# Kernel tuning notes

Measured on AMD Instinct MI355X. Metric: run time of the kernel, lower is better.

The kernel has to match this reference:

```python
import jax, jax.numpy as jnp
import numpy as np

N, E, G = 50000, 800000, 128          # nodes, edges, graphs
L, T, F = 4, 4, 20                    # conv layers, towers, per-tower width
D = T * F                             # 80 = hidden dim
EDGE_DIM = 16
AVG_DEG_LOG = float(np.log(17.0))     # avg_deg['log'] for avg in-degree ~16
EPS_STD = 1e-5
EPS_BN = 1e-5


def setup_inputs() -> dict:
    ks = iter(jax.random.split(jax.random.key(0), 32))
    rn = lambda *s: jax.random.normal(next(ks), s, jnp.float32) * 0.1
    return dict(
        x=jax.random.randint(next(ks), (N, 9), 0, 16),
        edge_index=jax.random.randint(next(ks), (2, E), 0, N),
        batch=jnp.sort(jax.random.randint(next(ks), (N,), 0, G)),
        edge_attr=rn(E, EDGE_DIM),
        atom_emb=rn(9, 16, D),
        edge_w=rn(L, EDGE_DIM, F), edge_b=jnp.zeros((L, F), jnp.float32),
        pre_w1=rn(L, T, 3 * F, F), pre_b1=jnp.zeros((L, T, F), jnp.float32),
        pre_w2=rn(L, T, F, F), pre_b2=jnp.zeros((L, T, F), jnp.float32),
        post_w1=rn(L, T, 13 * F, F), post_b1=jnp.zeros((L, T, F), jnp.float32),
        post_w2=rn(L, T, F, F), post_b2=jnp.zeros((L, T, F), jnp.float32),
        lin_w=rn(L, D, D), lin_b=jnp.zeros((L, D), jnp.float32),
        bn_g=jnp.ones((L, D), jnp.float32), bn_b=jnp.zeros((L, D), jnp.float32),
        mlp_w1=rn(D, 40), mlp_b1=jnp.zeros(40, jnp.float32),
        mlp_w2=rn(40, 20), mlp_b2=jnp.zeros(20, jnp.float32),
        mlp_w3=rn(20, 1), mlp_b3=jnp.zeros(1, jnp.float32),
    )


def _net(x, edge_index, batch, edge_attr, atom_emb, edge_w, edge_b, pre_w1,
         pre_b1, pre_w2, pre_b2, post_w1, post_b1, post_w2, post_b2, lin_w,
         lin_b, bn_g, bn_b, mlp_w1, mlp_b1, mlp_w2, mlp_b2, mlp_w3, mlp_b3):
    src, dst = edge_index[0], edge_index[1]
    # AtomEncoder: sum of 9 categorical embeddings -> [N, D]
    h = atom_emb[jnp.arange(9)[None, :], x].sum(1)
    deg_raw = jax.ops.segment_sum(jnp.ones((E,), jnp.float32), dst, N)
    deg = jnp.clip(deg_raw, 1.0)
    has_edge = (deg_raw > 0)[:, None, None]
    d3 = deg[:, None, None]
    logd = jnp.log(deg + 1.0)[:, None, None]
    for l in range(L):  # 4 PNAConv + BN + ReLU + residual (dropout off / eval)
        xt = h.reshape(N, T, F)
        ea = edge_attr @ edge_w[l] + edge_b[l]                      # [E, F]
        # message: concat(x_i, x_j, edge) -> per-tower pre MLP
        m = jnp.concatenate([xt[dst], xt[src],
                             jnp.broadcast_to(ea[:, None, :], (E, T, F))], -1)
        m = jax.nn.relu(jnp.einsum('eti,tio->eto', m, pre_w1[l]) + pre_b1[l])
        m = jnp.einsum('eti,tio->eto', m, pre_w2[l]) + pre_b2[l]    # [E,T,F]
        # multi-aggregator scatter-reduce
        mean = jax.ops.segment_sum(m, dst, N) / d3
        msq = jax.ops.segment_sum(m * m, dst, N) / d3
        std = jnp.sqrt(jax.nn.relu(msq - mean * mean) + EPS_STD)
        mn = jnp.where(has_edge, jax.ops.segment_min(m, dst, N), 0.0)
        mx = jnp.where(has_edge, jax.ops.segment_max(m, dst, N), 0.0)
        agg = jnp.concatenate([mean, mn, mx, std], -1)              # [N,T,4F]
        # degree scalers: identity, amplification, attenuation
        out = jnp.concatenate([agg, agg * (logd / AVG_DEG_LOG),
                               agg * (AVG_DEG_LOG / logd)], -1)     # [N,T,12F]
        out = jnp.concatenate([xt, out], -1)                        # [N,T,13F]
        out = jax.nn.relu(jnp.einsum('nti,tio->nto', out, post_w1[l]) + post_b1[l])
        out = jnp.einsum('nti,tio->nto', out, post_w2[l]) + post_b2[l]
        out = out.reshape(N, D) @ lin_w[l] + lin_b[l]
        # BatchNorm over nodes (batch statistics)
        mu = out.mean(0)
        var = jnp.mean((out - mu) ** 2, axis=0)
        out = (out - mu) * (bn_g[l] / jnp.sqrt(var + EPS_BN)) + bn_b[l]
        h = jax.nn.relu(out) + h
    # global mean pool over graphs + readout MLP
    cnt = jnp.clip(jax.ops.segment_sum(jnp.ones((N,), jnp.float32), batch, G), 1.0)
    g = jax.ops.segment_sum(h, batch, G) / cnt[:, None]
    g = jax.nn.relu(g @ mlp_w1 + mlp_b1)
    g = jax.nn.relu(g @ mlp_w2 + mlp_b2)
    return g @ mlp_w3 + mlp_b3                                      # [G, 1]


def reference(x, edge_index, batch, edge_attr, atom_emb, edge_w, edge_b, pre_w1,
              pre_b1, pre_w2, pre_b2, post_w1, post_b1, post_w2, post_b2, lin_w,
              lin_b, bn_g, bn_b, mlp_w1, mlp_b1, mlp_w2, mlp_b2, mlp_w3, mlp_b3):
    return _net(x, edge_index, batch, edge_attr, atom_emb, edge_w, edge_b, pre_w1,
                pre_b1, pre_w2, pre_b2, post_w1, post_b1, post_w2, post_b2,
                lin_w, lin_b, bn_g, bn_b, mlp_w1, mlp_b1, mlp_w2, mlp_b2,
                mlp_w3, mlp_b3)
```

## Files before the change

### kernel.cpp

```cpp
#include <hip/hip_runtime.h>
#include <hip/hip_bf16.h>

#define NN 50000
#define EE 800000
#define GG 128
#define LL 4
#define TT 4
#define FF 20
#define DD 80
#define SCAN_B ((NN + 1023) / 1024)
static constexpr float AVG_LOG = 2.8332133440562162f;

typedef __fp16 half2v __attribute__((ext_vector_type(2)));

__device__ __forceinline__ float bf2f(unsigned short u) {
  return __uint_as_float((unsigned)u << 16);
}
__device__ __forceinline__ unsigned short f2bf(float f) {
  __hip_bfloat16 b = __float2bfloat16(f);
  return *(unsigned short*)&b;
}
__device__ __forceinline__ half2v pkrtz(float a, float b) {
#if __has_builtin(__builtin_amdgcn_cvt_pkrtz)
  return __builtin_amdgcn_cvt_pkrtz(a, b);
#else
  half2v h; h.x = (__fp16)a; h.y = (__fp16)b; return h;
#endif
}
__device__ __forceinline__ float fdot2(half2v a, half2v b, float c) {
#if __has_builtin(__builtin_amdgcn_fdot2)
  return __builtin_amdgcn_fdot2(a, b, c, false);
#else
  return fmaf((float)a.x, (float)b.x, fmaf((float)a.y, (float)b.y, c));
#endif
}
__device__ __forceinline__ half2v u2h2(unsigned int u) {
  return __builtin_bit_cast(half2v, u);
}
__device__ __forceinline__ unsigned int h22u(half2v h) {
  return __builtin_bit_cast(unsigned int, h);
}
__device__ __forceinline__ unsigned int packh2_rne(float a, float b) {
  half2v h; h.x = (__fp16)a; h.y = (__fp16)b;
  return h22u(h);
}
__device__ __forceinline__ unsigned int pack_bf16(float a, float b) {
  return (unsigned int)f2bf(a) | ((unsigned int)f2bf(b) << 16);
}

__global__ __launch_bounds__(256) void k_h(const int* __restrict__ x,
                                           const float* __restrict__ atom_emb,
                                           float* __restrict__ h) {
  int idx = blockIdx.x * 256 + threadIdx.x;
  if (idx >= NN * DD) return;
  int n = idx / DD, d = idx - n * DD;
  const int* xr = x + n * 9;
  float acc = 0.f;
#pragma unroll
  for (int i = 0; i < 9; ++i) {
    int v = xr[i];
    acc += atom_emb[(i * 16 + v) * DD + d];
  }
  h[idx] = acc;
}

__global__ __launch_bounds__(256) void k_deg(const int* __restrict__ ei, int* __restrict__ cnt) {
  int e = blockIdx.x * 256 + threadIdx.x;
  if (e >= EE) return;
  atomicAdd(&cnt[ei[EE + e]], 1);
}

__global__ __launch_bounds__(1024) void k_scan_sum(const int* __restrict__ cnt, int* __restrict__ bsum) {
  __shared__ int red[1024];
  int tid = threadIdx.x;
  int i = blockIdx.x * 1024 + tid;
  red[tid] = (i < NN) ? cnt[i] : 0;
  __syncthreads();
  for (int off = 512; off > 0; off >>= 1) {
    if (tid < off) red[tid] += red[tid + off];
    __syncthreads();
  }
  if (tid == 0) bsum[blockIdx.x] = red[0];
}

__global__ void k_scan_top(const int* __restrict__ bsum, int* __restrict__ boff,
                           int* __restrict__ row_ptr) {
  if (threadIdx.x == 0 && blockIdx.x == 0) {
    int acc = 0;
    for (int b = 0; b < SCAN_B; ++b) { boff[b] = acc; acc += bsum[b]; }
    row_ptr[NN] = acc;
  }
}

__global__ __launch_bounds__(1024) void k_scan_apply(const int* __restrict__ cnt,
                                                     const int* __restrict__ boff,
                                                     int* __restrict__ row_ptr,
                                                     int* __restrict__ cursor) {
  __shared__ int sm[1024];
  int tid = threadIdx.x;
  int i = blockIdx.x * 1024 + tid;
  int v = (i < NN) ? cnt[i] : 0;
  sm[tid] = v;
  __syncthreads();
  for (int off = 1; off < 1024; off <<= 1) {
    int t = (tid >= off) ? sm[tid - off] : 0;
    __syncthreads();
    sm[tid] += t;
    __syncthreads();
  }
  int excl = boff[blockIdx.x] + sm[tid] - v;
  if (i < NN) { row_ptr[i] = excl; cursor[i] = excl; }
}

__global__ __launch_bounds__(256) void k_csrfill(const int* __restrict__ ei,
                                                 int* __restrict__ cursor,
                                                 int2* __restrict__ csr2,
                                                 int* __restrict__ csr_dst) {
  int e = blockIdx.x * 256 + threadIdx.x;
  if (e >= EE) return;
  int dst = ei[EE + e];
  int slot = atomicAdd(&cursor[dst], 1);
  csr2[slot] = make_int2(ei[e], e);
  csr_dst[slot] = dst;
}

__global__ __launch_bounds__(256) void k_nodeparams(const int* __restrict__ cnt,
                                                    float* __restrict__ inv_deg,
                                                    float* __restrict__ s1a,
                                                    float* __restrict__ s2a) {
  int n = blockIdx.x * 256 + threadIdx.x;
  if (n >= NN) return;
  int c = cnt[n];
  float deg = (c > 0) ? (float)c : 1.0f;
  inv_deg[n] = 1.0f / deg;
  float logd = logf(deg + 1.0f);
  s1a[n] = logd / AVG_LOG;
  s2a[n] = AVG_LOG / logd;
}

__global__ __launch_bounds__(64) void k_wcomb(const float* __restrict__ edge_w,
                                              const float* __restrict__ edge_b,
                                              const float* __restrict__ pre_w1,
                                              const float* __restrict__ pre_b1,
                                              const float* __restrict__ pre_w2,
                                              unsigned int* __restrict__ wcpk,
                                              unsigned int* __restrict__ w2pk,
                                              float* __restrict__ biasc, int l) {
  int t = blockIdx.x;
  int wt = l * TT + t;
  const float* W1 = pre_w1 + (size_t)wt * 1200;
  const float* W2 = pre_w2 + (size_t)wt * 400;
  const float* ew = edge_w + (size_t)l * 16 * FF;
  const float* eb = edge_b + (size_t)l * FF;
  int j = threadIdx.x;
  if (j >= FF) return;
  float col[16];
  for (int i = 0; i < 16; ++i) {
    float acc = 0.f;
#pragma unroll
    for (int f = 0; f < FF; ++f) acc = fmaf(ew[i * FF + f], W1[(40 + f) * FF + j], acc);
    col[i] = acc;
  }
#pragma unroll
  for (int i2 = 0; i2 < 8; ++i2)
    wcpk[((size_t)t * FF + j) * 8 + i2] = packh2_rne(col[2 * i2], col[2 * i2 + 1]);
#pragma unroll
  for (int i2 = 0; i2 < 10; ++i2)
    w2pk[((size_t)t * FF + j) * 10 + i2] = packh2_rne(W2[(2 * i2) * FF + j], W2[(2 * i2 + 1) * FF + j]);
  float b = pre_b1[wt * FF + j];
#pragma unroll
  for (int f = 0; f < FF; ++f) b = fmaf(eb[f], W1[(40 + f) * FF + j], b);
  biasc[t * FF + j] = b;
}

__global__ __launch_bounds__(256) void k_prenode(
    const float* __restrict__ h, const float* __restrict__ pre_w1,
    const float* __restrict__ biasc,
    unsigned short* __restrict__ predD, unsigned short* __restrict__ predS, int l) {
  int tid = threadIdx.x;
  int t = tid >> 6, lane = tid & 63;
  int n = blockIdx.x * 64 + lane;
  if (n >= NN) return;
  int wt_u = __builtin_amdgcn_readfirstlane(l * TT + t);
  const float* W1 = pre_w1 + (size_t)wt_u * 1200;
  const float* bc = biasc + t * FF;
  float xt[FF];
  {
    const float4* pp = (const float4*)(h + (size_t)n * DD + t * FF);
#pragma unroll
    for (int i = 0; i < 5; ++i) { float4 v = pp[i]; xt[i*4]=v.x; xt[i*4+1]=v.y; xt[i*4+2]=v.z; xt[i*4+3]=v.w; }
  }
  float d[FF], s[FF];
#pragma unroll
  for (int j = 0; j < FF; ++j) { d[j] = bc[j]; s[j] = 0.f; }
#pragma unroll
  for (int i = 0; i < FF; ++i) {
    float a = xt[i];
#pragma unroll
    for (int j = 0; j < FF; ++j) {
      d[j] = fmaf(a, W1[i * FF + j], d[j]);
      s[j] = fmaf(a, W1[(FF + i) * FF + j], s[j]);
    }
  }
  ushort4* pd = (ushort4*)(predD + (size_t)n * DD + t * FF);
  ushort4* ps = (ushort4*)(predS + (size_t)n * DD + t * FF);
#pragma unroll
  for (int i = 0; i < 5; ++i) {
    pd[i] = make_ushort4(f2bf(d[i*4]), f2bf(d[i*4+1]), f2bf(d[i*4+2]), f2bf(d[i*4+3]));
    ps[i] = make_ushort4(f2bf(s[i*4]), f2bf(s[i*4+1]), f2bf(s[i*4+2]), f2bf(s[i*4+3]));
  }
}

__global__ __launch_bounds__(256, 4) void k_pre(
    const unsigned short* __restrict__ predD, const unsigned short* __restrict__ predS,
    const float* __restrict__ edge_attr,
    const int2* __restrict__ csr2, const int* __restrict__ csr_dst,
    const int* __restrict__ row_ptr,
    const unsigned int* __restrict__ wcpk,
    const unsigned int* __restrict__ w2pk,
    const float* __restrict__ pre_b2,
    unsigned int* __restrict__ m, int l, int n0, int n1, int capSlots) {
  int tid = threadIdx.x;
  int t = tid >> 6;
  int lane = tid & 63;
  int wt_u = __builtin_amdgcn_readfirstlane(l * TT + t);
  int t_u  = __builtin_amdgcn_readfirstlane(t);
  const unsigned int* Wcp = wcpk + (size_t)t_u * FF * 8;
  const unsigned int* W2p = w2pk + (size_t)t_u * FF * 10;
  const float* b2 = pre_b2 + (size_t)wt_u * FF;

  int sl = blockIdx.x * 64 + lane;
  int base = row_ptr[n0], end = row_ptr[n1];
  if (sl >= capSlots || base + sl >= end) return;
  int p = base + sl;
  int2 se = csr2[p];
  int dst = csr_dst[p];

  float m1[FF];
  {
    const ushort4* pp = (const ushort4*)(predD + (size_t)dst * DD + t * FF);
    const ushort4* qq = (const ushort4*)(predS + (size_t)se.x * DD + t * FF);
#pragma unroll
    for (int i = 0; i < 5; ++i) {
      ushort4 u = pp[i];
      ushort4 v = qq[i];
      m1[i*4+0] = bf2f(u.x) + bf2f(v.x);
      m1[i*4+1] = bf2f(u.y) + bf2f(v.y);
      m1[i*4+2] = bf2f(u.z) + bf2f(v.z);
      m1[i*4+3] = bf2f(u.w) + bf2f(v.w);
    }
  }
  half2v eap[8];
  {
    const float4* ap = (const float4*)(edge_attr + (size_t)se.y * 16);
#pragma unroll
    for (int i = 0; i < 4; ++i) {
      float4 v = ap[i];
      eap[2*i]   = pkrtz(v.x, v.y);
      eap[2*i+1] = pkrtz(v.z, v.w);
    }
  }
#pragma unroll
  for (int j = 0; j < FF; ++j) {
    float c = m1[j];
#pragma unroll
    for (int i2 = 0; i2 < 8; ++i2) c = fdot2(eap[i2], u2h2(Wcp[j * 8 + i2]), c);
    m1[j] = c;
  }
  half2v mp[10];
#pragma unroll
  for (int pr = 0; pr < 10; ++pr)
    mp[pr] = pkrtz(fmaxf(m1[2*pr], 0.f), fmaxf(m1[2*pr+1], 0.f));
  float m2[FF];
#pragma unroll
  for (int j = 0; j < FF; ++j) {
    float c = b2[j];
#pragma unroll
    for (int i2 = 0; i2 < 10; ++i2) c = fdot2(mp[i2], u2h2(W2p[j * 10 + i2]), c);
    m2[j] = c;
  }
  unsigned int* mrow = m + (size_t)t * 10 * capSlots + sl;
#pragma unroll
  for (int pr = 0; pr < 10; ++pr)
    mrow[(size_t)pr * capSlots] = h22u(pkrtz(m2[2*pr], m2[2*pr+1]));
}

__global__ __launch_bounds__(320) void k_agg(
    const unsigned int* __restrict__ m,
    const int* __restrict__ row_ptr,
    const float* __restrict__ inv_deg,
    unsigned short* __restrict__ aggbuf, int n0, int n1, int capSlots) {
  int tid = threadIdx.x;
  int t = blockIdx.x & 3, tile = blockIdx.x >> 2;
  int ni = tid / 10, pr = tid - ni * 10;
  int n = n0 + tile * 32 + ni;
  if (n >= n1) return;
  int base = row_ptr[n0];
  int beg = row_ptr[n], end = row_ptr[n + 1];
  float inv = inv_deg[n];
  int s0 = beg - base, s1c = end - base;
  if (s0 < 0) s0 = 0;
  if (s1c > capSlots) s1c = capSlots;
  float sum0 = 0.f, sum1 = 0.f, sq0 = 0.f, sq1 = 0.f;
  float mn0 = 3.4e38f, mn1 = 3.4e38f, mx0 = -3.4e38f, mx1 = -3.4e38f;
  const unsigned int* mrow = m + (size_t)(t * 10 + pr) * capSlots;
  int p = s0;
  for (; p < s1c && (p & 3); ++p) {
    half2v h = u2h2(mrow[p]);
    float v0 = (float)h.x, v1 = (float)h.y;
    sum0 += v0; sq0 = fmaf(v0, v0, sq0); mn0 = fminf(mn0, v0); mx0 = fmaxf(mx0, v0);
    sum1 += v1; sq1 = fmaf(v1, v1, sq1); mn1 = fminf(mn1, v1); mx1 = fmaxf(mx1, v1);
  }
  for (; p + 4 <= s1c; p += 4) {
    uint4 q = *(const uint4*)(mrow + p);
#pragma unroll
    for (int k = 0; k < 4; ++k) {
      unsigned int u = (k == 0) ? q.x : (k == 1) ? q.y : (k == 2) ? q.z : q.w;
      half2v h = u2h2(u);
      float v0 = (float)h.x, v1 = (float)h.y;
      sum0 += v0; sq0 = fmaf(v0, v0, sq0); mn0 = fminf(mn0, v0); mx0 = fmaxf(mx0, v0);
      sum1 += v1; sq1 = fmaf(v1, v1, sq1); mn1 = fminf(mn1, v1); mx1 = fmaxf(mx1, v1);
    }
  }
  for (; p < s1c; ++p) {
    half2v h = u2h2(mrow[p]);
    float v0 = (float)h.x, v1 = (float)h.y;
    sum0 += v0; sq0 = fmaf(v0, v0, sq0); mn0 = fminf(mn0, v0); mx0 = fmaxf(mx0, v0);
    sum1 += v1; sq1 = fmaf(v1, v1, sq1); mn1 = fminf(mn1, v1); mx1 = fmaxf(mx1, v1);
  }
  float mu0 = sum0 * inv, mu1 = sum1 * inv;
  float sd0 = sqrtf(fmaxf(sq0 * inv - mu0 * mu0, 0.f) + 1e-5f);
  float sd1 = sqrtf(fmaxf(sq1 * inv - mu1 * mu1, 0.f) + 1e-5f);
  if (end <= beg) { mn0 = 0.f; mn1 = 0.f; mx0 = 0.f; mx1 = 0.f; }
  unsigned short* ab = aggbuf + ((size_t)(n - n0) * 4 + t) * 80;
  ((unsigned int*)(ab))[pr]      = pack_bf16(mu0, mu1);
  ((unsigned int*)(ab + 20))[pr] = pack_bf16(mn0, mn1);
  ((unsigned int*)(ab + 40))[pr] = pack_bf16(mx0, mx1);
  ((unsigned int*)(ab + 60))[pr] = pack_bf16(sd0, sd1);
}

__global__ __launch_bounds__(256) void k_post2(
    const float* __restrict__ h, const unsigned short* __restrict__ aggbuf,
    const float* __restrict__ s1a, const float* __restrict__ s2a,
    const float* __restrict__ post_w1, const float* __restrict__ post_b1,
    const float* __restrict__ post_w2, const float* __restrict__ post_b2,
    float* __restrict__ out2, int l, int n0, int n1) {
  int tid = threadIdx.x;
  int t = tid >> 6, lane = tid & 63;
  int wt_u = __builtin_amdgcn_readfirstlane(l * TT + t);
  const float* Q1 = post_w1 + (size_t)wt_u * 5200;
  const float* Q2 = post_w2 + (size_t)wt_u * 400;
  const float* B1 = post_b1 + (size_t)wt_u * FF;
  const float* B2 = post_b2 + (size_t)wt_u * FF;
  int n = n0 + blockIdx.x * 64 + lane;
  if (n >= n1) return;
  float c1 = s1a[n], c2 = s2a[n];
  float o1[FF];
#pragma unroll
  for (int j = 0; j < FF; ++j) o1[j] = B1[j];
  const float* hrow = h + (size_t)n * DD + t * FF;
  for (int i = 0; i < FF; ++i) {
    float a = hrow[i];
#pragma unroll
    for (int j = 0; j < FF; ++j) o1[j] = fmaf(a, Q1[i * FF + j], o1[j]);
  }
  const unsigned short* ab = aggbuf + ((size_t)(n - n0) * 4 + t) * 80;
  for (int i = 0; i < 80; ++i) {
    float a0 = bf2f(ab[i]);
    float a1 = a0 * c1, a2 = a0 * c2;
    int r = FF + i;
#pragma unroll
    for (int j = 0; j < FF; ++j) o1[j] = fmaf(a0, Q1[r * FF + j], o1[j]);
#pragma unroll
    for (int j = 0; j < FF; ++j) o1[j] = fmaf(a1, Q1[(r + 80) * FF + j], o1[j]);
#pragma unroll
    for (int j = 0; j < FF; ++j) o1[j] = fmaf(a2, Q1[(r + 160) * FF + j], o1[j]);
  }
#pragma unroll
  for (int j = 0; j < FF; ++j) o1[j] = fmaxf(o1[j], 0.f);
  float o2[FF];
#pragma unroll
  for (int j = 0; j < FF; ++j) o2[j] = B2[j];
#pragma unroll
  for (int i = 0; i < FF; ++i) {
    float a = o1[i];
#pragma unroll
    for (int j = 0; j < FF; ++j) o2[j] = fmaf(a, Q2[i * FF + j], o2[j]);
  }
  float4* op = (float4*)(out2 + (size_t)n * DD + t * FF);
#pragma unroll
  for (int i = 0; i < 5; ++i) op[i] = make_float4(o2[i*4], o2[i*4+1], o2[i*4+2], o2[i*4+3]);
}

__global__ __launch_bounds__(320) void k_lin(const float* __restrict__ out2,
                                             const float* __restrict__ lin_w,
                                             const float* __restrict__ lin_b,
                                             float* __restrict__ outl,
                                             float* __restrict__ colsum, int l) {
  __shared__ float Wl[DD * DD];
  __shared__ float rowbuf[4 * DD];
  __shared__ float red[320];
  int tid = threadIdx.x;
  for (int i = tid; i < DD * DD; i += 320) Wl[i] = lin_w[(size_t)l * DD * DD + i];
  __syncthreads();
  int nl = tid / DD, d = tid - nl * DD;
  float bias = lin_b[l * DD + d];
  float bsum = 0.f, bsq = 0.f;
  for (int base = blockIdx.x * 4; base < NN; base += gridDim.x * 4) {
    int gi = base * DD + tid;
    rowbuf[tid] = (gi < NN * DD) ? out2[gi] : 0.f;
    __syncthreads();
    int n = base + nl;
    if (n < NN) {
      float acc = bias;
#pragma unroll
      for (int i = 0; i < DD; ++i) acc = fmaf(rowbuf[nl * DD + i], Wl[i * DD + d], acc);
      outl[(size_t)n * DD + d] = acc;
      bsum += acc; bsq += acc * acc;
    }
    __syncthreads();
  }
  red[tid] = bsum;
  __syncthreads();
  if (tid < DD) {
    float s = red[tid] + red[tid + DD] + red[tid + 2 * DD] + red[tid + 3 * DD];
    atomicAdd(&colsum[d], s);
  }
  __syncthreads();
  red[tid] = bsq;
  __syncthreads();
  if (tid < DD) {
    float s = red[tid] + red[tid + DD] + red[tid + 2 * DD] + red[tid + 3 * DD];
    atomicAdd(&colsum[DD + d], s);
  }
}

__global__ __launch_bounds__(128) void k_bnfinal(const float* __restrict__ colsum,
                                                 const float* __restrict__ bn_g,
                                                 const float* __restrict__ bn_b,
                                                 float* __restrict__ bnsc, int l) {
  int d = threadIdx.x;
  if (d >= DD) return;
  float mu = colsum[d] * (1.0f / NN);
  float var = colsum[DD + d] * (1.0f / NN) - mu * mu;
  float sc = bn_g[l * DD + d] * rsqrtf(var + 1e-5f);
  bnsc[d] = sc;
  bnsc[DD + d] = bn_b[l * DD + d] - mu * sc;
}

__global__ __launch_bounds__(256) void k_bnapply(const float* __restrict__ outl,
                                                 const float* __restrict__ bnsc,
                                                 float* __restrict__ h) {
  int idx = blockIdx.x * 256 + threadIdx.x;
  if (idx >= NN * DD) return;
  int d = idx % DD;
  float v = fmaf(outl[idx], bnsc[d], bnsc[DD + d]);
  h[idx] += fmaxf(v, 0.f);
}

__global__ __launch_bounds__(256) void k_gcnt(const int* __restrict__ batch, int* __restrict__ gcnt) {
  __shared__ int hcnt[GG];
  int tid = threadIdx.x;
  if (tid < GG) hcnt[tid] = 0;
  __syncthreads();
  int n = blockIdx.x * 256 + tid;
  if (n < NN) atomicAdd(&hcnt[batch[n]], 1);
  __syncthreads();
  if (tid < GG && hcnt[tid] > 0) atomicAdd(&gcnt[tid], hcnt[tid]);
}

__global__ void k_gstart(const int* __restrict__ gcnt, int* __restrict__ gstart) {
  if (threadIdx.x == 0 && blockIdx.x == 0) {
    int acc = 0;
    for (int g = 0; g < GG; ++g) { gstart[g] = acc; acc += gcnt[g]; }
  }
}

__global__ __launch_bounds__(320) void k_gmean(const float* __restrict__ h,
                                               const int* __restrict__ gstart,
                                               const int* __restrict__ gcnt,
                                               float* __restrict__ gbuf) {
  __shared__ float red[320];
  int g = blockIdx.x, tid = threadIdx.x;
  int nl = tid / DD, d = tid - nl * DD;
  int start = gstart[g], c = gcnt[g];
  float acc = 0.f;
  for (int r = start + nl; r < start + c; r += 4) acc += h[(size_t)r * DD + d];
  red[tid] = acc;
  __syncthreads();
  if (tid < DD) {
    float s = red[tid] + red[tid + DD] + red[tid + 2 * DD] + red[tid + 3 * DD];
    float cf = (c > 0) ? (float)c : 1.0f;
    gbuf[g * DD + tid] = s / cf;
  }
}

__global__ __launch_bounds__(64) void k_mlp(const float* __restrict__ gbuf,
                                            const float* __restrict__ w1, const float* __restrict__ b1,
                                            const float* __restrict__ w2, const float* __restrict__ b2,
                                            const float* __restrict__ w3, const float* __restrict__ b3,
                                            float* __restrict__ out) {
  __shared__ float row[DD];
  __shared__ float t1[40];
  __shared__ float t2[20];
  int g = blockIdx.x, tid = threadIdx.x;
  for (int i = tid; i < DD; i += 64) row[i] = gbuf[g * DD + i];
  __syncthreads();
  if (tid < 40) {
    float acc = b1[tid];
#pragma unroll
    for (int i = 0; i < DD; ++i) acc = fmaf(row[i], w1[i * 40 + tid], acc);
    t1[tid] = fmaxf(acc, 0.f);
  }
  __syncthreads();
  if (tid < 20) {
    float acc = b2[tid];
#pragma unroll
    for (int i = 0; i < 40; ++i) acc = fmaf(t1[i], w2[i * 20 + tid], acc);
    t2[tid] = fmaxf(acc, 0.f);
  }
  __syncthreads();
  if (tid == 0) {
    float acc = b3[0];
#pragma unroll
    for (int i = 0; i < 20; ++i) acc = fmaf(t2[i], w3[i], acc);
    out[g] = acc;
  }
}

extern "C" void kernel_launch(void* const* d_in, const int* in_sizes, int n_in,
                              void* d_out, int out_size, void* d_ws, size_t ws_size,
                              hipStream_t stream) {
  const int*   x         = (const int*)d_in[0];
  const int*   ei        = (const int*)d_in[1];
  const int*   batch     = (const int*)d_in[2];
  const float* edge_attr = (const float*)d_in[3];
  const float* atom_emb  = (const float*)d_in[4];
  const float* edge_w    = (const float*)d_in[5];
  const float* edge_b    = (const float*)d_in[6];
  const float* pre_w1    = (const float*)d_in[7];
  const float* pre_b1    = (const float*)d_in[8];
  const float* pre_w2    = (const float*)d_in[9];
  const float* pre_b2    = (const float*)d_in[10];
  const float* post_w1   = (const float*)d_in[11];
  const float* post_b1   = (const float*)d_in[12];
  const float* post_w2   = (const float*)d_in[13];
  const float* post_b2   = (const float*)d_in[14];
  const float* lin_w     = (const float*)d_in[15];
  const float* lin_b     = (const float*)d_in[16];
  const float* bn_g      = (const float*)d_in[17];
  const float* bn_b      = (const float*)d_in[18];
  const float* mlp_w1    = (const float*)d_in[19];
  const float* mlp_b1    = (const float*)d_in[20];
  const float* mlp_w2    = (const float*)d_in[21];
  const float* mlp_b2    = (const float*)d_in[22];
  const float* mlp_w3    = (const float*)d_in[23];
  const float* mlp_b3    = (const float*)d_in[24];
  float* out = (float*)d_out;

  char* ws = (char*)d_ws;
  size_t off = 0;
  auto alloc = [&](size_t bytes) -> void* {
    void* p = ws + off;
    off += (bytes + 15) & ~(size_t)15;
    return p;
  };
  float* h       = (float*)alloc((size_t)NN * DD * 4);
  float* out2    = (float*)alloc((size_t)NN * DD * 4);
  unsigned short* predD = (unsigned short*)alloc((size_t)NN * DD * 2);
  unsigned short* predS = (unsigned short*)alloc((size_t)NN * DD * 2);
  int2*  csr2    = (int2*)alloc((size_t)EE * 8);
  int*   csr_dst = (int*)alloc((size_t)EE * 4);
  int*   row_ptr = (int*)alloc((size_t)(NN + 1) * 4);
  int*   cnt     = (int*)alloc((size_t)NN * 4);
  int*   cursor  = (int*)alloc((size_t)NN * 4);
  float* inv_deg = (float*)alloc((size_t)NN * 4);
  float* s1a     = (float*)alloc((size_t)NN * 4);
  float* s2a     = (float*)alloc((size_t)NN * 4);
  float* colsum  = (float*)alloc(2 * DD * 4);
  float* bnsc    = (float*)alloc(2 * DD * 4);
  float* gbuf    = (float*)alloc((size_t)GG * DD * 4);
  unsigned int* wcpk  = (unsigned int*)alloc((size_t)TT * FF * 8 * 4);
  unsigned int* w2pk  = (unsigned int*)alloc((size_t)TT * FF * 10 * 4);
  float* biasc   = (float*)alloc((size_t)TT * FF * 4);
  int*   bsum    = (int*)alloc((size_t)SCAN_B * 4);
  int*   boff    = (int*)alloc((size_t)SCAN_B * 4);
  int*   gcnt    = (int*)alloc((size_t)GG * 4);
  int*   gstart  = (int*)alloc((size_t)(GG + 1) * 4);
  (void)in_sizes; (void)n_in; (void)out_size;

  size_t rest = (ws_size > off) ? (ws_size - off) : 0;
  static const int cands[] = {1, 2, 4, 5, 8, 10, 20, 25, 40, 50};
  int c = -1, capSlots = 0, nodesPer = 0;
  size_t aggBytes = 0;
  for (int ci = 0; ci < 10; ++ci) {
    int cc = cands[ci];
    int np = (NN + cc - 1) / cc;
    size_t ab = ((size_t)np * 4 * 80 * 2 + 63) & ~(size_t)63;
    int slots = EE / cc + 25000; if (slots > EE) slots = EE;
    slots = (slots + 63) & ~63;
    size_t mb = (size_t)slots * DD * 2;
    if (ab + mb <= rest && ab + mb >= (size_t)NN * DD * 4) {
      c = cc; capSlots = slots; nodesPer = np; aggBytes = ab;
      break;
    }
  }
  if (c < 0) {
    c = 50; nodesPer = (NN + c - 1) / c;
    aggBytes = ((size_t)nodesPer * 4 * 80 * 2 + 63) & ~(size_t)63;
    size_t mb = (rest > aggBytes) ? rest - aggBytes : 0;
    capSlots = (int)(mb / (DD * 2)) & ~63;
  }
  unsigned short* aggbuf = (unsigned short*)(ws + off);
  unsigned int* mbuf = (unsigned int*)(ws + off + aggBytes);
  float* outl = (float*)(ws + off);

  hipMemsetAsync(cnt, 0, (size_t)NN * 4, stream);
  k_h<<<(NN * DD + 255) / 256, 256, 0, stream>>>(x, atom_emb, h);
  k_deg<<<(EE + 255) / 256, 256, 0, stream>>>(ei, cnt);
  k_scan_sum<<<SCAN_B, 1024, 0, stream>>>(cnt, bsum);
  k_scan_top<<<1, 64, 0, stream>>>(bsum, boff, row_ptr);
  k_scan_apply<<<SCAN_B, 1024, 0, stream>>>(cnt, boff, row_ptr, cursor);
  k_csrfill<<<(EE + 255) / 256, 256, 0, stream>>>(ei, cursor, csr2, csr_dst);
  k_nodeparams<<<(NN + 255) / 256, 256, 0, stream>>>(cnt, inv_deg, s1a, s2a);

  for (int l = 0; l < LL; ++l) {
    k_wcomb<<<TT, 64, 0, stream>>>(edge_w, edge_b, pre_w1, pre_b1, pre_w2, wcpk, w2pk, biasc, l);
    k_prenode<<<(NN + 63) / 64, 256, 0, stream>>>(h, pre_w1, biasc, predD, predS, l);
    for (int ck = 0; ck < c; ++ck) {
      int n0 = ck * nodesPer;
      int n1 = n0 + nodesPer; if (n1 > NN) n1 = NN;
      if (n0 >= n1) continue;
      int preBlocks = (capSlots + 63) / 64;
      k_pre<<<preBlocks, 256, 0, stream>>>(predD, predS, edge_attr, csr2, csr_dst, row_ptr,
          wcpk, w2pk, pre_b2, mbuf, l, n0, n1, capSlots);
      int aggBlocks = ((n1 - n0 + 31) / 32) * 4;
      k_agg<<<aggBlocks, 320, 0, stream>>>(mbuf, row_ptr, inv_deg, aggbuf, n0, n1, capSlots);
      int p2Blocks = (n1 - n0 + 63) / 64;
      k_post2<<<p2Blocks, 256, 0, stream>>>(h, aggbuf, s1a, s2a,
          post_w1, post_b1, post_w2, post_b2, out2, l, n0, n1);
    }
    hipMemsetAsync(colsum, 0, 2 * DD * 4, stream);
    k_lin<<<512, 320, 0, stream>>>(out2, lin_w, lin_b, outl, colsum, l);
    k_bnfinal<<<1, 128, 0, stream>>>(colsum, bn_g, bn_b, bnsc, l);
    k_bnapply<<<(NN * DD + 255) / 256, 256, 0, stream>>>(outl, bnsc, h);
  }

  hipMemsetAsync(gcnt, 0, (size_t)GG * 4, stream);
  k_gcnt<<<(NN + 255) / 256, 256, 0, stream>>>(batch, gcnt);
  k_gstart<<<1, 64, 0, stream>>>(gcnt, gstart);
  k_gmean<<<GG, 320, 0, stream>>>(h, gstart, gcnt, gbuf);
  k_mlp<<<GG, 64, 0, stream>>>(gbuf, mlp_w1, mlp_b1, mlp_w2, mlp_b2, mlp_w3, mlp_b3, out);
}
```

Before: 1.550 ms.

## Use packed fp16 dot2 weights in post-MLP and make tower block-uniform

Adds a per-layer kernel that packs the post_w1 aggregate rows and post_w2 into fp16 pairs. k_post2 then does those matmuls with fdot2 on packed fp16 activations, which halves the FMA count. The grid is also remapped so each block handles a single tower over 256 nodes, so weight loads stay uniform across the block. Feature and aggregate rows are now loaded with vector loads. In exchange, activations and weights drop to fp16 precision (the degree scalers are multiplied in fp16), and one extra small kernel launch is added per layer.

```diff
diff --git a/kernel.cpp b/kernel.cpp
--- a/kernel.cpp
+++ b/kernel.cpp
@@ -171,6 +171,26 @@
 #pragma unroll
   for (int f = 0; f < FF; ++f) b = fmaf(eb[f], W1[(40 + f) * FF + j], b);
   biasc[t * FF + j] = b;
+}
+
+__global__ __launch_bounds__(64) void k_postpk(const float* __restrict__ post_w1,
+                                               const float* __restrict__ post_w2,
+                                               unsigned int* __restrict__ q1pk,
+                                               unsigned int* __restrict__ q2pk, int l) {
+  int t = blockIdx.x;
+  int wt = l * TT + t;
+  const float* Q1 = post_w1 + (size_t)wt * 5200;
+  const float* Q2 = post_w2 + (size_t)wt * 400;
+  int j = threadIdx.x;
+  if (j >= FF) return;
+  for (int i2 = 0; i2 < 120; ++i2) {
+    int blk = i2 / 40, k = i2 - blk * 40;
+    int r0 = 20 + 80 * blk + 2 * k;
+    q1pk[((size_t)t * 120 + i2) * FF + j] = packh2_rne(Q1[r0 * FF + j], Q1[(r0 + 1) * FF + j]);
+  }
+#pragma unroll
+  for (int i2 = 0; i2 < 10; ++i2)
+    q2pk[((size_t)t * 10 + i2) * FF + j] = packh2_rne(Q2[(2 * i2) * FF + j], Q2[(2 * i2 + 1) * FF + j]);
 }
 
 __global__ __launch_bounds__(256) void k_prenode(
@@ -343,49 +363,86 @@
     const float* __restrict__ h, const unsigned short* __restrict__ aggbuf,
     const float* __restrict__ s1a, const float* __restrict__ s2a,
     const float* __restrict__ post_w1, const float* __restrict__ post_b1,
-    const float* __restrict__ post_w2, const float* __restrict__ post_b2,
-    float* __restrict__ out2, int l, int n0, int n1) {
-  int tid = threadIdx.x;
-  int t = tid >> 6, lane = tid & 63;
-  int wt_u = __builtin_amdgcn_readfirstlane(l * TT + t);
+    const unsigned int* __restrict__ q1pk, const unsigned int* __restrict__ q2pk,
+    const float* __restrict__ post_b2,
+    float* __restrict__ out2, int l, int n0, int n1, int tiles) {
+  int t = blockIdx.x / tiles;
+  int tile = blockIdx.x - t * tiles;
+  int wt_u = l * TT + t;
   const float* Q1 = post_w1 + (size_t)wt_u * 5200;
-  const float* Q2 = post_w2 + (size_t)wt_u * 400;
   const float* B1 = post_b1 + (size_t)wt_u * FF;
   const float* B2 = post_b2 + (size_t)wt_u * FF;
-  int n = n0 + blockIdx.x * 64 + lane;
+  const unsigned int* q1 = q1pk + (size_t)t * 120 * FF;
+  const unsigned int* q2 = q2pk + (size_t)t * 10 * FF;
+  int n = n0 + tile * 256 + threadIdx.x;
   if (n >= n1) return;
   float c1 = s1a[n], c2 = s2a[n];
+  half2v c1p = pkrtz(c1, c1), c2p = pkrtz(c2, c2);
+  float xt[FF];
+  {
+    const float4* pp = (const float4*)(h + (size_t)n * DD + t * FF);
+#pragma unroll
+    for (int i = 0; i < 5; ++i) { float4 v = pp[i]; xt[i*4]=v.x; xt[i*4+1]=v.y; xt[i*4+2]=v.z; xt[i*4+3]=v.w; }
+  }
+  half2v a0p[40];
+  {
+    const uint4* ap = (const uint4*)(aggbuf + ((size_t)(n - n0) * 4 + t) * 80);
+#pragma unroll
+    for (int q = 0; q < 10; ++q) {
+      uint4 v = ap[q];
+      unsigned int w[4] = {v.x, v.y, v.z, v.w};
+#pragma unroll
+      for (int k = 0; k < 4; ++k) {
+        unsigned int u = w[k];
+        float lo = __uint_as_float(u << 16);
+        float hi = __uint_as_float(u & 0xffff0000u);
+        a0p[q * 4 + k] = pkrtz(lo, hi);
+      }
+    }
+  }
   float o1[FF];
 #pragma unroll
   for (int j = 0; j < FF; ++j) o1[j] = B1[j];
-  const float* hrow = h + (size_t)n * DD + t * FF;
+#pragma unroll
   for (int i = 0; i < FF; ++i) {
-    float a = hrow[i];
+    float a = xt[i];
 #pragma unroll
     for (int j = 0; j < FF; ++j) o1[j] = fmaf(a, Q1[i * FF + j], o1[j]);
   }
-  const unsigned short* ab = aggbuf + ((size_t)(n - n0) * 4 + t) * 80;
-  for (int i = 0; i < 80; ++i) {
-    float a0 = bf2f(ab[i]);
-    float a1 = a0 * c1, a2 = a0 * c2;
-    int r = FF + i;
-#pragma unroll
-    for (int j = 0; j < FF; ++j) o1[j] = fmaf(a0, Q1[r * FF + j], o1[j]);
-#pragma unroll
-    for (int j = 0; j < FF; ++j) o1[j] = fmaf(a1, Q1[(r + 80) * FF + j], o1[j]);
-#pragma unroll
-    for (int j = 0; j < FF; ++j) o1[j] = fmaf(a2, Q1[(r + 160) * FF + j], o1[j]);
-  }
-#pragma unroll
-  for (int j = 0; j < FF; ++j) o1[j] = fmaxf(o1[j], 0.f);
+#pragma unroll 2
+  for (int k = 0; k < 40; ++k) {
+    half2v act = a0p[k];
+    const unsigned int* wr = q1 + k * FF;
+#pragma unroll
+    for (int j = 0; j < FF; ++j) o1[j] = fdot2(act, u2h2(wr[j]), o1[j]);
+  }
+#pragma unroll 2
+  for (int k = 0; k < 40; ++k) {
+    half2v act = a0p[k] * c1p;
+    const unsigned int* wr = q1 + (40 + k) * FF;
+#pragma unroll
+    for (int j = 0; j < FF; ++j) o1[j] = fdot2(act, u2h2(wr[j]), o1[j]);
+  }
+#pragma unroll 2
+  for (int k = 0; k < 40; ++k) {
+    half2v act = a0p[k] * c2p;
+    const unsigned int* wr = q1 + (80 + k) * FF;
+#pragma unroll
+    for (int j = 0; j < FF; ++j) o1[j] = fdot2(act, u2h2(wr[j]), o1[j]);
+  }
+  half2v o1p[10];
+#pragma unroll
+  for (int i2 = 0; i2 < 10; ++i2)
+    o1p[i2] = pkrtz(fmaxf(o1[2*i2], 0.f), fmaxf(o1[2*i2+1], 0.f));
   float o2[FF];
 #pragma unroll
   for (int j = 0; j < FF; ++j) o2[j] = B2[j];
-#pragma unroll
-  for (int i = 0; i < FF; ++i) {
-    float a = o1[i];
-#pragma unroll
-    for (int j = 0; j < FF; ++j) o2[j] = fmaf(a, Q2[i * FF + j], o2[j]);
+#pragma unroll 2
+  for (int i2 = 0; i2 < 10; ++i2) {
+    half2v act = o1p[i2];
+    const unsigned int* wr = q2 + i2 * FF;
+#pragma unroll
+    for (int j = 0; j < FF; ++j) o2[j] = fdot2(act, u2h2(wr[j]), o2[j]);
   }
   float4* op = (float4*)(out2 + (size_t)n * DD + t * FF);
 #pragma unroll
@@ -582,6 +639,8 @@
   float* gbuf    = (float*)alloc((size_t)GG * DD * 4);
   unsigned int* wcpk  = (unsigned int*)alloc((size_t)TT * FF * 8 * 4);
   unsigned int* w2pk  = (unsigned int*)alloc((size_t)TT * FF * 10 * 4);
+  unsigned int* q1pk  = (unsigned int*)alloc((size_t)TT * 120 * FF * 4);
+  unsigned int* q2pk  = (unsigned int*)alloc((size_t)TT * 10 * FF * 4);
   float* biasc   = (float*)alloc((size_t)TT * FF * 4);
   int*   bsum    = (int*)alloc((size_t)SCAN_B * 4);
   int*   boff    = (int*)alloc((size_t)SCAN_B * 4);
@@ -626,6 +685,7 @@
 
   for (int l = 0; l < LL; ++l) {
     k_wcomb<<<TT, 64, 0, stream>>>(edge_w, edge_b, pre_w1, pre_b1, pre_w2, wcpk, w2pk, biasc, l);
+    k_postpk<<<TT, 64, 0, stream>>>(post_w1, post_w2, q1pk, q2pk, l);
     k_prenode<<<(NN + 63) / 64, 256, 0, stream>>>(h, pre_w1, biasc, predD, predS, l);
     for (int ck = 0; ck < c; ++ck) {
       int n0 = ck * nodesPer;
@@ -636,9 +696,9 @@
           wcpk, w2pk, pre_b2, mbuf, l, n0, n1, capSlots);
       int aggBlocks = ((n1 - n0 + 31) / 32) * 4;
       k_agg<<<aggBlocks, 320, 0, stream>>>(mbuf, row_ptr, inv_deg, aggbuf, n0, n1, capSlots);
-      int p2Blocks = (n1 - n0 + 63) / 64;
-      k_post2<<<p2Blocks, 256, 0, stream>>>(h, aggbuf, s1a, s2a,
-          post_w1, post_b1, post_w2, post_b2, out2, l, n0, n1);
+      int tiles = (n1 - n0 + 255) / 256;
+      k_post2<<<tiles * TT, 256, 0, stream>>>(h, aggbuf, s1a, s2a,
+          post_w1, post_b1, q1pk, q2pk, post_b2, out2, l, n0, n1, tiles);
     }
     hipMemsetAsync(colsum, 0, 2 * DD * 4, stream);
     k_lin<<<512, 320, 0, stream>>>(out2, lin_w, lin_b, outl, colsum, l);
```

Result: slower. 1.596 ms (+3.0%).
